# Optimization experiments

Hardware: AMD Instinct MI355X
Metric: run time of the kernel (lower is better)

The kernel has to match this reference:

```python
import jax, jax.numpy as jnp
import numpy as np
from jax import lax

EPS = 1e-5
DN = ('NCHW', 'OIHW', 'NCHW')

def ternarize(w):
    # TWN-style ternarization: delta = 0.7*mean|w|, alpha = mean of |w| above threshold
    a = jnp.abs(w)
    delta = 0.7 * jnp.mean(a)
    mask = (a > delta).astype(w.dtype)
    alpha = jnp.sum(a * mask) / jnp.maximum(jnp.sum(mask), 1.0)
    return alpha * jnp.sign(w) * mask

def conv(x, w, stride=1, pad=0, groups=1):
    return lax.conv_general_dilated(
        x, w, (stride, stride), [(pad, pad), (pad, pad)],
        feature_group_count=groups, dimension_numbers=DN)

def batchnorm(x, gamma, beta):
    # training-mode BN: per-channel batch statistics over (N,H,W)
    mean = jnp.mean(x, axis=(0, 2, 3), keepdims=True)
    var = jnp.var(x, axis=(0, 2, 3), keepdims=True)
    inv = lax.rsqrt(var + EPS)
    return (x - mean) * inv * gamma[None, :, None, None] + beta[None, :, None, None]

def setup_inputs() -> dict:
    key = jax.random.key(0)
    ks = jax.random.split(key, 10)
    B, Cin, H, W = 32, 96, 56, 56
    planes, Cout = 576, 96
    return {
        'x':  jax.random.normal(ks[0], (B, Cin, H, W), jnp.float32),
        'w1': jax.random.normal(ks[1], (planes, Cin, 1, 1), jnp.float32) * 0.1,
        'g1': jax.random.uniform(ks[2], (planes,), jnp.float32, 0.5, 1.5),
        'b1': jax.random.normal(ks[3], (planes,), jnp.float32) * 0.1,
        'w2': jax.random.normal(ks[4], (planes, 1, 3, 3), jnp.float32) * 0.1,
        'g2': jax.random.uniform(ks[5], (planes,), jnp.float32, 0.5, 1.5),
        'b2': jax.random.normal(ks[6], (planes,), jnp.float32) * 0.1,
        'w3': jax.random.normal(ks[7], (Cout, planes, 1, 1), jnp.float32) * 0.1,
        'g3': jax.random.uniform(ks[8], (Cout,), jnp.float32, 0.5, 1.5),
        'b3': jax.random.normal(ks[9], (Cout,), jnp.float32) * 0.1,
    }

def reference(x, w1, g1, b1, w2, g2, b2, w3, g3, b3):
    planes = w1.shape[0]
    # expand 1x1 (ternary) + BN + ReLU
    out = jax.nn.relu(batchnorm(conv(x, ternarize(w1)), g1, b1))
    # depthwise 3x3 stride 1 (ternary) + BN + ReLU
    out = jax.nn.relu(batchnorm(conv(out, ternarize(w2), stride=1, pad=1, groups=planes), g2, b2))
    # project 1x1 (ternary) + BN
    out = batchnorm(conv(out, ternarize(w3)), g3, b3)
    # stride==1 and in_planes==out_planes -> identity shortcut
    return out + x
```

## Files before the change

kernel.cpp:

```cpp
#include <hip/hip_runtime.h>
#include <hip/hip_bf16.h>

#define BATCH 32
#define CIN 96
#define HW 3136
#define PL 576
#define COUT 96
#define NT 49
#define NHW 100352.0

typedef __attribute__((ext_vector_type(4))) float f32x4;
typedef __attribute__((ext_vector_type(8))) short s16x8;

__device__ __forceinline__ unsigned short f2b(float v) {
  __hip_bfloat16 h = __float2bfloat16(v);
  return *reinterpret_cast<unsigned short*>(&h);
}
__device__ __forceinline__ float b2f(unsigned int u) {
  return __uint_as_float((u & 0xffffu) << 16);
}

__global__ __launch_bounds__(256) void absred_kernel(const float* __restrict__ w,
                                                     float* __restrict__ part, int n4) {
  __shared__ float ra[256];
  const int tid = threadIdx.x;
  float s = 0.f;
  for (int i = blockIdx.x * 256 + tid; i < n4; i += 32 * 256) {
    float4 v = reinterpret_cast<const float4*>(w)[i];
    s += fabsf(v.x) + fabsf(v.y) + fabsf(v.z) + fabsf(v.w);
  }
  ra[tid] = s; __syncthreads();
  for (int off = 128; off; off >>= 1) { if (tid < off) ra[tid] += ra[tid + off]; __syncthreads(); }
  if (tid == 0) part[blockIdx.x] = ra[0];
}

__device__ __forceinline__ float delta_from_parts(const float* __restrict__ part, float invn) {
  float s = 0.f;
#pragma unroll
  for (int i = 0; i < 32; ++i) s += part[i];
  return 0.7f * s * invn;
}

__global__ __launch_bounds__(256) void ternw_bf16_kernel(
    const float* __restrict__ w, const float* __restrict__ part, float invn,
    __hip_bfloat16* __restrict__ tw, int n4) {
  const float delta = delta_from_parts(part, invn);
  const int i = blockIdx.x * 256 + threadIdx.x;
  if (i >= n4) return;
  float4 v = reinterpret_cast<const float4*>(w)[i];
  float vv[4] = {v.x, v.y, v.z, v.w};
  unsigned short b[4];
#pragma unroll
  for (int j = 0; j < 4; ++j)
    b[j] = (fabsf(vv[j]) > delta)
               ? (unsigned short)(0x3F80u | ((__float_as_uint(vv[j]) >> 16) & 0x8000u))
               : (unsigned short)0;
  unsigned lo = (unsigned)b[0] | ((unsigned)b[1] << 16);
  unsigned hi = (unsigned)b[2] | ((unsigned)b[3] << 16);
  reinterpret_cast<uint2*>(tw)[i] = make_uint2(lo, hi);
}

__global__ __launch_bounds__(256) void ternw_f32_kernel(
    const float* __restrict__ w, const float* __restrict__ part, float invn,
    float* __restrict__ tw, int n4) {
  const float delta = delta_from_parts(part, invn);
  const int i = blockIdx.x * 256 + threadIdx.x;
  if (i >= n4) return;
  float4 v = reinterpret_cast<const float4*>(w)[i];
  float4 o;
  o.x = (fabsf(v.x) > delta) ? (v.x > 0.f ? 1.f : -1.f) : 0.f;
  o.y = (fabsf(v.y) > delta) ? (v.y > 0.f ? 1.f : -1.f) : 0.f;
  o.z = (fabsf(v.z) > delta) ? (v.z > 0.f ? 1.f : -1.f) : 0.f;
  o.w = (fabsf(v.w) > delta) ? (v.w > 0.f ? 1.f : -1.f) : 0.f;
  reinterpret_cast<float4*>(tw)[i] = o;
}

__global__ __launch_bounds__(256) void bnp_kernel(
    const float* __restrict__ psum, const float* __restrict__ psumsq,
    const float* __restrict__ gamma, const float* __restrict__ beta,
    float* __restrict__ sc, float* __restrict__ sh, int nparts) {
  const int ch = blockIdx.x, tid = threadIdx.x;
  double s = 0.0, q = 0.0;
  for (int i = tid; i < nparts; i += 256) {
    s += (double)psum[(size_t)ch * nparts + i];
    q += (double)psumsq[(size_t)ch * nparts + i];
  }
  __shared__ double rs[256], rq[256];
  rs[tid] = s; rq[tid] = q; __syncthreads();
  for (int off = 128; off; off >>= 1) {
    if (tid < off) { rs[tid] += rs[tid + off]; rq[tid] += rq[tid + off]; }
    __syncthreads();
  }
  if (tid == 0) {
    double mean = rs[0] / NHW;
    double var = rq[0] / NHW - mean * mean;
    float inv = (float)(1.0 / sqrt(var + 1e-5));
    float g = gamma[ch];
    sc[ch] = inv * g;
    sh[ch] = beta[ch] - (float)mean * inv * g;
  }
}

__global__ __launch_bounds__(256) void conv1_mfma(
    const float* __restrict__ x, const __hip_bfloat16* __restrict__ tw1,
    __hip_bfloat16* __restrict__ o1c,
    float* __restrict__ psum, float* __restrict__ psumsq) {
  __shared__ __hip_bfloat16 Bt[64 * 104];
  __shared__ __hip_bfloat16 ot[64 * 200];
  const int hwt = blockIdx.x, n = blockIdx.y, mt = blockIdx.z;
  const int t0 = hwt * 64;
  const int tid = threadIdx.x;
  const int lane = tid & 63, w = tid >> 6;

  {
    const float* xp = x + (size_t)n * CIN * HW + t0 + lane;
    const int cb = w * 24;
#pragma unroll
    for (int i6 = 0; i6 < 6; ++i6) {
      const int c0 = cb + i6 * 4;
      float v0 = xp[(size_t)(c0 + 0) * HW];
      float v1 = xp[(size_t)(c0 + 1) * HW];
      float v2 = xp[(size_t)(c0 + 2) * HW];
      float v3 = xp[(size_t)(c0 + 3) * HW];
      unsigned lo = (unsigned)f2b(v0) | ((unsigned)f2b(v1) << 16);
      unsigned hi = (unsigned)f2b(v2) | ((unsigned)f2b(v3) << 16);
      *reinterpret_cast<uint2*>(&Bt[lane * 104 + c0]) = make_uint2(lo, hi);
    }
  }
  __syncthreads();

  const int l15 = lane & 15, lh = lane >> 4;
  f32x4 acc[3][4];
#pragma unroll
  for (int f = 0; f < 3; ++f)
#pragma unroll
    for (int g = 0; g < 4; ++g) acc[f][g] = (f32x4){0.f, 0.f, 0.f, 0.f};
  const int rowb = mt * 192 + w * 48;
#pragma unroll
  for (int k0 = 0; k0 < 3; ++k0) {
    s16x8 a[3], b[4];
#pragma unroll
    for (int f = 0; f < 3; ++f)
      a[f] = *reinterpret_cast<const s16x8*>(tw1 + (size_t)(rowb + f * 16 + l15) * CIN + k0 * 32 + lh * 8);
#pragma unroll
    for (int g = 0; g < 4; ++g)
      b[g] = *reinterpret_cast<const s16x8*>(&Bt[(g * 16 + l15) * 104 + k0 * 32 + lh * 8]);
#pragma unroll
    for (int f = 0; f < 3; ++f)
#pragma unroll
      for (int g = 0; g < 4; ++g)
        acc[f][g] = __builtin_amdgcn_mfma_f32_16x16x32_bf16(a[f], b[g], acc[f][g], 0, 0, 0);
  }

#pragma unroll
  for (int f = 0; f < 3; ++f) {
    float sred[4] = {0.f, 0.f, 0.f, 0.f};
    float qred[4] = {0.f, 0.f, 0.f, 0.f};
    const int ch0 = rowb + f * 16 + lh * 4;
#pragma unroll
    for (int g = 0; g < 4; ++g)
#pragma unroll
      for (int r = 0; r < 4; ++r) {
        float v = acc[f][g][r];
        sred[r] += v; qred[r] = fmaf(v, v, qred[r]);
      }
#pragma unroll
    for (int r = 0; r < 4; ++r) {
      float s = sred[r], q = qred[r];
#pragma unroll
      for (int m = 1; m < 16; m <<= 1) { s += __shfl_xor(s, m); q += __shfl_xor(q, m); }
      if (l15 == 0) {
        const int pi = (ch0 + r) * 1568 + n * NT + hwt;
        psum[pi] = s; psumsq[pi] = q;
      }
    }
  }

#pragma unroll
  for (int f = 0; f < 3; ++f) {
    const int chL = w * 48 + f * 16 + lh * 4;
#pragma unroll
    for (int g = 0; g < 4; ++g) {
      unsigned p0 = (unsigned)f2b(acc[f][g][0]) | ((unsigned)f2b(acc[f][g][1]) << 16);
      unsigned p1 = (unsigned)f2b(acc[f][g][2]) | ((unsigned)f2b(acc[f][g][3]) << 16);
      *reinterpret_cast<uint2*>(&ot[(g * 16 + l15) * 200 + chL]) = make_uint2(p0, p1);
    }
  }
  __syncthreads();

  {
    const int hwp = tid >> 2, q = tid & 3;
    const __hip_bfloat16* src = &ot[hwp * 200];
    __hip_bfloat16* dst = o1c + ((size_t)n * HW + t0 + hwp) * PL + mt * 192;
#pragma unroll
    for (int s = 0; s < 6; ++s) {
      const int c8 = q + s * 4;
      *reinterpret_cast<uint4*>(dst + c8 * 8) =
          *reinterpret_cast<const uint4*>(src + c8 * 8);
    }
  }
}

__global__ __launch_bounds__(64) void dw_kernel(
    const __hip_bfloat16* __restrict__ o1c, const float* __restrict__ tw2,
    const float* __restrict__ s1, const float* __restrict__ t1,
    __hip_bfloat16* __restrict__ o2c,
    float* __restrict__ psum, float* __restrict__ psumsq) {
  const int strip = blockIdx.x, kh = blockIdx.y, n = blockIdx.z;
  const int lane = threadIdx.x;
  const int col = lane >> 4, chs = lane & 15;
  const int c = strip * 4 + col;
  const int chb = kh * 64 + chs * 4;
  const int ec = (col == 0) ? (c - 1) : (c + 1);
  const bool eok = (col == 0) ? (c > 0) : ((col == 3) ? (c < 55) : false);

  float sc[4], sh[4], wt[9][4];
#pragma unroll
  for (int j = 0; j < 4; ++j) {
    sc[j] = s1[chb + j]; sh[j] = t1[chb + j];
#pragma unroll
    for (int t = 0; t < 9; ++t) wt[t][j] = tw2[(chb + j) * 9 + t];
  }

  const size_t nb = (size_t)n * HW;
  const __hip_bfloat16* pc = o1c + (nb + c) * PL + chb;
  const __hip_bfloat16* pe = o1c + (nb + ((eok ? ec : c))) * PL + chb;
  __hip_bfloat16* po = o2c + (nb + c) * PL + chb;

  uint2 rc[8], re[8];
  float Wl[4][4], Wc[4][4], Wr[4][4];
  float psc[4] = {0.f, 0.f, 0.f, 0.f}, psq[4] = {0.f, 0.f, 0.f, 0.f};

#define LOADRAW(s, q_) do {                                                    \
    rc[s] = make_uint2(0u, 0u); re[s] = make_uint2(0u, 0u);                    \
    if ((q_) < 56) {                                                           \
      rc[s] = *reinterpret_cast<const uint2*>(pc + (size_t)(q_) * 56 * PL);    \
      if (eok) re[s] = *reinterpret_cast<const uint2*>(pe + (size_t)(q_) * 56 * PL); \
    } } while (0)

#define BN4(dst, raw) do {                                                     \
    dst[0] = fmaxf(fmaf(b2f((raw).x), sc[0], sh[0]), 0.f);                     \
    dst[1] = fmaxf(fmaf(b2f((raw).x >> 16), sc[1], sh[1]), 0.f);               \
    dst[2] = fmaxf(fmaf(b2f((raw).y), sc[2], sh[2]), 0.f);                     \
    dst[3] = fmaxf(fmaf(b2f((raw).y >> 16), sc[3], sh[3]), 0.f);               \
  } while (0)

#define CONVW(wi, s, q_) do {                                                  \
    if ((q_) < 56) {                                                           \
      float cen_[4], ee_[4];                                                   \
      BN4(cen_, rc[s]); BN4(ee_, re[s]);                                       \
      _Pragma("unroll")                                                        \
      for (int j = 0; j < 4; ++j) {                                            \
        float lv = __shfl(cen_[j], lane - 16);                                 \
        float rv = __shfl(cen_[j], lane + 16);                                 \
        float ev = eok ? ee_[j] : 0.f;                                         \
        Wc[wi][j] = cen_[j];                                                   \
        Wl[wi][j] = (col == 0) ? ev : lv;                                      \
        Wr[wi][j] = (col == 3) ? ev : rv;                                      \
      }                                                                        \
    } else {                                                                   \
      _Pragma("unroll")                                                        \
      for (int j = 0; j < 4; ++j) { Wl[wi][j] = 0.f; Wc[wi][j] = 0.f; Wr[wi][j] = 0.f; } \
    } } while (0)

#define COMPW(qm, q0, qp, q_) do {                                             \
    float o_[4];                                                               \
    _Pragma("unroll")                                                          \
    for (int j = 0; j < 4; ++j) {                                              \
      float a_ = wt[0][j] * Wl[qm][j];                                         \
      a_ = fmaf(wt[1][j], Wc[qm][j], a_);                                      \
      a_ = fmaf(wt[2][j], Wr[qm][j], a_);                                      \
      a_ = fmaf(wt[3][j], Wl[q0][j], a_);                                      \
      a_ = fmaf(wt[4][j], Wc[q0][j], a_);                                      \
      a_ = fmaf(wt[5][j], Wr[q0][j], a_);                                      \
      a_ = fmaf(wt[6][j], Wl[qp][j], a_);                                      \
      a_ = fmaf(wt[7][j], Wc[qp][j], a_);                                      \
      a_ = fmaf(wt[8][j], Wr[qp][j], a_);                                      \
      o_[j] = a_;                                                              \
      psc[j] += a_; psq[j] = fmaf(a_, a_, psq[j]);                             \
    }                                                                          \
    unsigned pk0 = (unsigned)f2b(o_[0]) | ((unsigned)f2b(o_[1]) << 16);        \
    unsigned pk1 = (unsigned)f2b(o_[2]) | ((unsigned)f2b(o_[3]) << 16);        \
    *reinterpret_cast<uint2*>(po + (size_t)(q_) * 56 * PL) = make_uint2(pk0, pk1); \
  } while (0)

  LOADRAW(0, 0); LOADRAW(1, 1); LOADRAW(2, 2); LOADRAW(3, 3);
  LOADRAW(4, 4); LOADRAW(5, 5); LOADRAW(6, 6); LOADRAW(7, 7);
  CONVW(0, 0, 0);
#pragma unroll
  for (int j = 0; j < 4; ++j) { Wl[3][j] = 0.f; Wc[3][j] = 0.f; Wr[3][j] = 0.f; }

  for (int t = 0; t < 7; ++t) {
    const int q = 8 * t;
    LOADRAW(0, q + 8);  CONVW(1, 1, q + 1);  COMPW(3, 0, 1, q);
    LOADRAW(1, q + 9);  CONVW(2, 2, q + 2);  COMPW(0, 1, 2, q + 1);
    LOADRAW(2, q + 10); CONVW(3, 3, q + 3);  COMPW(1, 2, 3, q + 2);
    LOADRAW(3, q + 11); CONVW(0, 4, q + 4);  COMPW(2, 3, 0, q + 3);
    LOADRAW(4, q + 12); CONVW(1, 5, q + 5);  COMPW(3, 0, 1, q + 4);
    LOADRAW(5, q + 13); CONVW(2, 6, q + 6);  COMPW(0, 1, 2, q + 5);
    LOADRAW(6, q + 14); CONVW(3, 7, q + 7);  COMPW(1, 2, 3, q + 6);
    LOADRAW(7, q + 15); CONVW(0, 0, q + 8);  COMPW(2, 3, 0, q + 7);
  }
#undef COMPW
#undef CONVW
#undef BN4
#undef LOADRAW

#pragma unroll
  for (int j = 0; j < 4; ++j) {
    psc[j] += __shfl_xor(psc[j], 16); psc[j] += __shfl_xor(psc[j], 32);
    psq[j] += __shfl_xor(psq[j], 16); psq[j] += __shfl_xor(psq[j], 32);
  }
  if (col == 0) {
#pragma unroll
    for (int j = 0; j < 4; ++j) {
      const int pi = (chb + j) * 448 + n * 14 + strip;
      psum[pi] = psc[j]; psumsq[pi] = psq[j];
    }
  }
}

__global__ __launch_bounds__(256) void conv3_mfma(
    const __hip_bfloat16* __restrict__ o2c, const __hip_bfloat16* __restrict__ tw3,
    const float* __restrict__ s2, const float* __restrict__ t2,
    __hip_bfloat16* __restrict__ out3,
    float* __restrict__ psum, float* __restrict__ psumsq) {
  __shared__ __hip_bfloat16 chunk[2][64 * 64];
  __shared__ float smem[96 * 65];
  __shared__ float s2s[PL], t2s[PL];
  const int hwt = blockIdx.x, n = blockIdx.y, tid = threadIdx.x;
  const int lane = tid & 63, w = tid >> 6;
  const int l15 = lane & 15, lh = lane >> 4;
  const int wm = w >> 1, wn = w & 1;
  const int t0 = hwt * 64;
  for (int i = tid; i < PL; i += 256) { s2s[i] = s2[i]; t2s[i] = t2[i]; }

  const int hwp = tid >> 2;
  const int cq = tid & 3;
  const __hip_bfloat16* src = o2c + ((size_t)n * HW + t0 + hwp) * PL + cq * 16;
  uint4 ra = *reinterpret_cast<const uint4*>(src);
  uint4 rb = *reinterpret_cast<const uint4*>(src + 8);

  f32x4 acc[3][2];
#pragma unroll
  for (int f = 0; f < 3; ++f)
#pragma unroll
    for (int g = 0; g < 2; ++g) acc[f][g] = (f32x4){0.f, 0.f, 0.f, 0.f};

  const unsigned key = (unsigned)((hwp & 7) << 4);
  __syncthreads();

  for (int kc = 0; kc < 9; ++kc) {
    const int cur = kc & 1;
    {
      const int cb16 = kc * 64 + cq * 16;
      unsigned uu[8] = {ra.x, ra.y, ra.z, ra.w, rb.x, rb.y, rb.z, rb.w};
      unsigned po[8];
#pragma unroll
      for (int j = 0; j < 8; ++j) {
        float lo = fmaxf(fmaf(b2f(uu[j]),       s2s[cb16 + 2 * j],     t2s[cb16 + 2 * j]), 0.f);
        float hi = fmaxf(fmaf(b2f(uu[j] >> 16), s2s[cb16 + 2 * j + 1], t2s[cb16 + 2 * j + 1]), 0.f);
        po[j] = (unsigned)f2b(lo) | ((unsigned)f2b(hi) << 16);
      }
      char* base = (char*)&chunk[cur][0] + hwp * 128;
      *reinterpret_cast<uint4*>(base + (((unsigned)(cq * 32)) ^ key)) =
          make_uint4(po[0], po[1], po[2], po[3]);
      *reinterpret_cast<uint4*>(base + (((unsigned)(cq * 32 + 16)) ^ key)) =
          make_uint4(po[4], po[5], po[6], po[7]);
    }
    __syncthreads();
    if (kc < 8) {
      ra = *reinterpret_cast<const uint4*>(src + (kc + 1) * 64);
      rb = *reinterpret_cast<const uint4*>(src + (kc + 1) * 64 + 8);
    }
#pragma unroll
    for (int kb = 0; kb < 2; ++kb) {
      s16x8 a[3];
#pragma unroll
      for (int f = 0; f < 3; ++f)
        a[f] = *reinterpret_cast<const s16x8*>(
            tw3 + (size_t)(wm * 48 + f * 16 + l15) * PL + kc * 64 + kb * 32 + lh * 8);
#pragma unroll
      for (int g = 0; g < 2; ++g) {
        const int row = wn * 32 + g * 16 + l15;
        const unsigned cbyte = (unsigned)(kb * 64 + lh * 16) ^ (unsigned)((row & 7) << 4);
        const s16x8 b = *reinterpret_cast<const s16x8*>(
            (const char*)&chunk[cur][0] + row * 128 + cbyte);
#pragma unroll
        for (int f = 0; f < 3; ++f)
          acc[f][g] = __builtin_amdgcn_mfma_f32_16x16x32_bf16(a[f], b, acc[f][g], 0, 0, 0);
      }
    }
  }
  __syncthreads();
#pragma unroll
  for (int f = 0; f < 3; ++f)
#pragma unroll
    for (int g = 0; g < 2; ++g)
#pragma unroll
      for (int r = 0; r < 4; ++r)
        smem[(wm * 48 + f * 16 + lh * 4 + r) * 65 + wn * 32 + g * 16 + l15] = acc[f][g][r];
  __syncthreads();
  const int slot = tid & 7, rgrp = tid >> 3;
#pragma unroll
  for (int s = 0; s < 3; ++s) {
    const int rl = s * 32 + rgrp;
    float v[8], sm = 0.f, sq = 0.f;
#pragma unroll
    for (int j = 0; j < 8; ++j) {
      float t = smem[rl * 65 + slot * 8 + j];
      v[j] = t; sm += t; sq = fmaf(t, t, sq);
    }
    unsigned pk[4];
#pragma unroll
    for (int j = 0; j < 4; ++j) pk[j] = (unsigned)f2b(v[2 * j]) | ((unsigned)f2b(v[2 * j + 1]) << 16);
    *reinterpret_cast<uint4*>(out3 + ((size_t)n * COUT + rl) * HW + t0 + slot * 8) =
        make_uint4(pk[0], pk[1], pk[2], pk[3]);
#pragma unroll
    for (int m = 1; m < 8; m <<= 1) { sm += __shfl_xor(sm, m, 8); sq += __shfl_xor(sq, m, 8); }
    if (slot == 0) { int pi = rl * 1568 + n * NT + hwt; psum[pi] = sm; psumsq[pi] = sq; }
  }
}

__global__ __launch_bounds__(256) void final_kernel(
    const __hip_bfloat16* __restrict__ out3, const float* __restrict__ x,
    const float* __restrict__ s3, const float* __restrict__ t3,
    float* __restrict__ out) {
  const int i = blockIdx.x * 256 + threadIdx.x;
  const int p = (i * 4) / HW;
  const int co = p - (p / COUT) * COUT;
  uint2 raw = reinterpret_cast<const uint2*>(out3)[i];
  float4 b = reinterpret_cast<const float4*>(x)[i];
  const float scv = s3[co], tv = t3[co];
  float4 r;
  r.x = fmaf(b2f(raw.x), scv, tv) + b.x;
  r.y = fmaf(b2f(raw.x >> 16), scv, tv) + b.y;
  r.z = fmaf(b2f(raw.y), scv, tv) + b.z;
  r.w = fmaf(b2f(raw.y >> 16), scv, tv) + b.w;
  reinterpret_cast<float4*>(out)[i] = r;
}

extern "C" void kernel_launch(void* const* d_in, const int* in_sizes, int n_in,
                              void* d_out, int out_size, void* d_ws, size_t ws_size,
                              hipStream_t stream) {
  const float* x  = (const float*)d_in[0];
  const float* w1 = (const float*)d_in[1];
  const float* g1 = (const float*)d_in[2];
  const float* b1 = (const float*)d_in[3];
  const float* w2 = (const float*)d_in[4];
  const float* g2 = (const float*)d_in[5];
  const float* b2 = (const float*)d_in[6];
  const float* w3 = (const float*)d_in[7];
  const float* g3 = (const float*)d_in[8];
  const float* b3 = (const float*)d_in[9];
  float* out = (float*)d_out;

  char* ws = (char*)d_ws;
  __hip_bfloat16* tw1b = (__hip_bfloat16*)(ws + 0);
  __hip_bfloat16* tw3b = (__hip_bfloat16*)(ws + 110592);
  float* tw2f = (float*)(ws + 221184);
  float* s1 = (float*)(ws + 241920);
  float* t1 = s1 + PL; float* s2 = t1 + PL; float* t2 = s2 + PL;
  float* s3 = (float*)(ws + 251136); float* t3 = s3 + COUT;
  float* ps1 = (float*)(ws + 251904);
  float* pq1 = ps1 + PL * 1568;
  float* ps2 = pq1 + PL * 1568;
  float* pq2 = ps2 + PL * 1568;
  float* ps3 = pq2 + PL * 1568;
  float* pq3 = ps3 + COUT * 1568;
  float* part1 = pq3 + COUT * 1568;
  float* part2 = part1 + 32;
  float* part3 = part2 + 32;
  __hip_bfloat16* o1c = (__hip_bfloat16*)(ws + 16777216);
  __hip_bfloat16* o2c = o1c + (size_t)BATCH * HW * PL;
  __hip_bfloat16* out3b = o1c;

  absred_kernel<<<32, 256, 0, stream>>>(w1, part1, 13824);
  absred_kernel<<<32, 256, 0, stream>>>(w2, part2, 1296);
  absred_kernel<<<32, 256, 0, stream>>>(w3, part3, 13824);
  ternw_bf16_kernel<<<54, 256, 0, stream>>>(w1, part1, 1.0f / 55296.0f, tw1b, 13824);
  ternw_f32_kernel <<<6, 256, 0, stream>>>(w2, part2, 1.0f / 5184.0f, tw2f, 1296);
  ternw_bf16_kernel<<<54, 256, 0, stream>>>(w3, part3, 1.0f / 55296.0f, tw3b, 13824);

  conv1_mfma<<<dim3(NT, BATCH, 3), 256, 0, stream>>>(x, tw1b, o1c, ps1, pq1);
  bnp_kernel<<<PL, 256, 0, stream>>>(ps1, pq1, g1, b1, s1, t1, 1568);

  dw_kernel<<<dim3(14, 9, BATCH), 64, 0, stream>>>(o1c, tw2f, s1, t1, o2c, ps2, pq2);
  bnp_kernel<<<PL, 256, 0, stream>>>(ps2, pq2, g2, b2, s2, t2, 448);

  conv3_mfma<<<dim3(NT, BATCH), 256, 0, stream>>>(o2c, tw3b, s2, t2, out3b, ps3, pq3);
  bnp_kernel<<<COUT, 256, 0, stream>>>(ps3, pq3, g3, b3, s3, t3, 1568);

  final_kernel<<<out_size / 1024, 256, 0, stream>>>(out3b, x, s3, t3, out);
}
```

Baseline: 236.9 us.

## Load conv3 B operands straight from global per wave, dropping LDS staging

The projection kernel no longer stages the BN2+ReLU-transformed depthwise output through a double-buffered, swizzled LDS tile with per-chunk block barriers. Each wave now owns 16 spatial positions and all 96 output channels. It loads its B fragments directly from global memory with a 3-deep register prefetch and applies the scale, shift and ReLU in registers before the MFMA. The conv1 writeback is also reshaped so 8 threads cover each row, which gives more contiguous stores. This removes the LDS traffic and barriers, but each lane now does a 16-byte strided global load per k-step, and the ternary weight loads are no longer shared across waves.

```diff
diff --git a/kernel.cpp b/kernel.cpp
--- a/kernel.cpp
+++ b/kernel.cpp
@@ -189,14 +189,18 @@
   __syncthreads();
 
   {
-    const int hwp = tid >> 2, q = tid & 3;
-    const __hip_bfloat16* src = &ot[hwp * 200];
-    __hip_bfloat16* dst = o1c + ((size_t)n * HW + t0 + hwp) * PL + mt * 192;
-#pragma unroll
-    for (int s = 0; s < 6; ++s) {
-      const int c8 = q + s * 4;
-      *reinterpret_cast<uint4*>(dst + c8 * 8) =
-          *reinterpret_cast<const uint4*>(src + c8 * 8);
+    const int hwp = tid >> 3, q = tid & 7;
+#pragma unroll
+    for (int half = 0; half < 2; ++half) {
+      const int hw = half * 32 + hwp;
+      const __hip_bfloat16* srcp = &ot[hw * 200];
+      __hip_bfloat16* dst = o1c + ((size_t)n * HW + t0 + hw) * PL + mt * 192;
+#pragma unroll
+      for (int s = 0; s < 3; ++s) {
+        const int c8 = q + s * 8;
+        *reinterpret_cast<uint4*>(dst + c8 * 8) =
+            *reinterpret_cast<const uint4*>(srcp + c8 * 8);
+      }
     }
   }
 }
@@ -325,81 +329,60 @@
     const float* __restrict__ s2, const float* __restrict__ t2,
     __hip_bfloat16* __restrict__ out3,
     float* __restrict__ psum, float* __restrict__ psumsq) {
-  __shared__ __hip_bfloat16 chunk[2][64 * 64];
   __shared__ float smem[96 * 65];
   __shared__ float s2s[PL], t2s[PL];
   const int hwt = blockIdx.x, n = blockIdx.y, tid = threadIdx.x;
   const int lane = tid & 63, w = tid >> 6;
   const int l15 = lane & 15, lh = lane >> 4;
-  const int wm = w >> 1, wn = w & 1;
   const int t0 = hwt * 64;
   for (int i = tid; i < PL; i += 256) { s2s[i] = s2[i]; t2s[i] = t2[i]; }
-
-  const int hwp = tid >> 2;
-  const int cq = tid & 3;
-  const __hip_bfloat16* src = o2c + ((size_t)n * HW + t0 + hwp) * PL + cq * 16;
-  uint4 ra = *reinterpret_cast<const uint4*>(src);
-  uint4 rb = *reinterpret_cast<const uint4*>(src + 8);
-
-  f32x4 acc[3][2];
-#pragma unroll
-  for (int f = 0; f < 3; ++f)
-#pragma unroll
-    for (int g = 0; g < 2; ++g) acc[f][g] = (f32x4){0.f, 0.f, 0.f, 0.f};
-
-  const unsigned key = (unsigned)((hwp & 7) << 4);
   __syncthreads();
 
-  for (int kc = 0; kc < 9; ++kc) {
-    const int cur = kc & 1;
-    {
-      const int cb16 = kc * 64 + cq * 16;
-      unsigned uu[8] = {ra.x, ra.y, ra.z, ra.w, rb.x, rb.y, rb.z, rb.w};
-      unsigned po[8];
-#pragma unroll
-      for (int j = 0; j < 8; ++j) {
-        float lo = fmaxf(fmaf(b2f(uu[j]),       s2s[cb16 + 2 * j],     t2s[cb16 + 2 * j]), 0.f);
-        float hi = fmaxf(fmaf(b2f(uu[j] >> 16), s2s[cb16 + 2 * j + 1], t2s[cb16 + 2 * j + 1]), 0.f);
-        po[j] = (unsigned)f2b(lo) | ((unsigned)f2b(hi) << 16);
-      }
-      char* base = (char*)&chunk[cur][0] + hwp * 128;
-      *reinterpret_cast<uint4*>(base + (((unsigned)(cq * 32)) ^ key)) =
-          make_uint4(po[0], po[1], po[2], po[3]);
-      *reinterpret_cast<uint4*>(base + (((unsigned)(cq * 32 + 16)) ^ key)) =
-          make_uint4(po[4], po[5], po[6], po[7]);
-    }
-    __syncthreads();
-    if (kc < 8) {
-      ra = *reinterpret_cast<const uint4*>(src + (kc + 1) * 64);
-      rb = *reinterpret_cast<const uint4*>(src + (kc + 1) * 64 + 8);
-    }
-#pragma unroll
-    for (int kb = 0; kb < 2; ++kb) {
-      s16x8 a[3];
-#pragma unroll
-      for (int f = 0; f < 3; ++f)
-        a[f] = *reinterpret_cast<const s16x8*>(
-            tw3 + (size_t)(wm * 48 + f * 16 + l15) * PL + kc * 64 + kb * 32 + lh * 8);
-#pragma unroll
-      for (int g = 0; g < 2; ++g) {
-        const int row = wn * 32 + g * 16 + l15;
-        const unsigned cbyte = (unsigned)(kb * 64 + lh * 16) ^ (unsigned)((row & 7) << 4);
-        const s16x8 b = *reinterpret_cast<const s16x8*>(
-            (const char*)&chunk[cur][0] + row * 128 + cbyte);
-#pragma unroll
-        for (int f = 0; f < 3; ++f)
-          acc[f][g] = __builtin_amdgcn_mfma_f32_16x16x32_bf16(a[f], b, acc[f][g], 0, 0, 0);
-      }
-    }
-  }
-  __syncthreads();
-#pragma unroll
-  for (int f = 0; f < 3; ++f)
-#pragma unroll
-    for (int g = 0; g < 2; ++g)
-#pragma unroll
-      for (int r = 0; r < 4; ++r)
-        smem[(wm * 48 + f * 16 + lh * 4 + r) * 65 + wn * 32 + g * 16 + l15] = acc[f][g][r];
+  const __hip_bfloat16* bsrc =
+      o2c + ((size_t)n * HW + t0 + w * 16 + l15) * PL + lh * 8;
+  f32x4 acc[6];
+#pragma unroll
+  for (int f = 0; f < 6; ++f) acc[f] = (f32x4){0.f, 0.f, 0.f, 0.f};
+
+  uint4 bq[3];
+  bq[0] = *reinterpret_cast<const uint4*>(bsrc);
+  bq[1] = *reinterpret_cast<const uint4*>(bsrc + 32);
+#pragma unroll
+  for (int it = 0; it < 18; ++it) {
+    const int slot = it % 3;
+    if (it + 2 < 18)
+      bq[(it + 2) % 3] = *reinterpret_cast<const uint4*>(bsrc + (it + 2) * 32);
+    const int cb = it * 32 + lh * 8;
+    const f32x4 sa = *reinterpret_cast<const f32x4*>(&s2s[cb]);
+    const f32x4 sb = *reinterpret_cast<const f32x4*>(&s2s[cb + 4]);
+    const f32x4 ta = *reinterpret_cast<const f32x4*>(&t2s[cb]);
+    const f32x4 tb = *reinterpret_cast<const f32x4*>(&t2s[cb + 4]);
+    const unsigned uu[4] = {bq[slot].x, bq[slot].y, bq[slot].z, bq[slot].w};
+    union BU { unsigned u[4]; s16x8 v; } bu;
+#pragma unroll
+    for (int j = 0; j < 4; ++j) {
+      const float svl = (j < 2) ? sa[2 * j] : sb[2 * (j - 2)];
+      const float svh = (j < 2) ? sa[2 * j + 1] : sb[2 * (j - 2) + 1];
+      const float tvl = (j < 2) ? ta[2 * j] : tb[2 * (j - 2)];
+      const float tvh = (j < 2) ? ta[2 * j + 1] : tb[2 * (j - 2) + 1];
+      float lo = fmaxf(fmaf(b2f(uu[j]), svl, tvl), 0.f);
+      float hi = fmaxf(fmaf(b2f(uu[j] >> 16), svh, tvh), 0.f);
+      bu.u[j] = (unsigned)f2b(lo) | ((unsigned)f2b(hi) << 16);
+    }
+    const s16x8 b = bu.v;
+#pragma unroll
+    for (int f = 0; f < 6; ++f) {
+      const s16x8 a = *reinterpret_cast<const s16x8*>(
+          tw3 + (size_t)(f * 16 + l15) * PL + it * 32 + lh * 8);
+      acc[f] = __builtin_amdgcn_mfma_f32_16x16x32_bf16(a, b, acc[f], 0, 0, 0);
+    }
+  }
+
+#pragma unroll
+  for (int f = 0; f < 6; ++f)
+#pragma unroll
+    for (int r = 0; r < 4; ++r)
+      smem[(f * 16 + lh * 4 + r) * 65 + w * 16 + l15] = acc[f][r];
   __syncthreads();
   const int slot = tid & 7, rgrp = tid >> 3;
 #pragma unroll
```

New measurement: 271.7 us. +14.7%, slower.
